# Performance work log

Measured on AMD Instinct MI355X. Metric: run time of the kernel, lower is better.

The kernel has to match this reference:

```python
import jax, jax.numpy as jnp
import numpy as np

EPS = 1e-6
LOSS_WEIGHT = 1.0


def _sigma_components(xywhr):
    """Closed-form symmetric 2x2 covariance Sigma = R diag((w/2)^2,(h/2)^2) R^T.
    Returns the three independent components (s00, s01, s11)."""
    wh = jnp.clip(xywhr[..., 2:4], 1e-7, 1e7)
    r = xywhr[..., 4]
    c, s = jnp.cos(r), jnp.sin(r)
    a = (0.5 * wh[..., 0]) ** 2  # (w/2)^2
    b = (0.5 * wh[..., 1]) ** 2  # (h/2)^2
    s00 = a * c * c + b * s * s
    s01 = (a - b) * s * c
    s11 = a * s * s + b * c * c
    return s00, s01, s11


def setup_inputs() -> dict:
    key = jax.random.key(0)
    kp, kt = jax.random.split(key)
    pred = jax.random.uniform(kp, (4096, 5), dtype=jnp.float32)
    target = jax.random.uniform(kt, (2048, 5), dtype=jnp.float32)
    return {"pred": pred, "target": target}


def reference(pred, target):
    # box_decode is identity here (boxes already xywhr). match=True path -> (M, N) cost.
    p00, p01, p11 = _sigma_components(pred)    # each (M,)
    t00, t01, t11 = _sigma_components(target)  # each (N,)

    det_p = p00 * p11 - p01 * p01
    det_t = t00 * t11 - t01 * t01
    Vb_p = 4.0 * jnp.sqrt(jnp.abs(det_p))[:, None]  # (M, 1)
    Vb_t = 4.0 * jnp.sqrt(jnp.abs(det_t))[None, :]  # (1, N)

    # Broadcast pred components over columns, target over rows -> (M, N) planes.
    p00, p01, p11 = p00[:, None], p01[:, None], p11[:, None]
    t00, t01, t11 = t00[None, :], t01[None, :], t11[None, :]

    # Sum S = Sigma_p + Sigma_t (symmetric), closed-form 2x2 inverse.
    m00, m01, m11 = p00 + t00, p01 + t01, p11 + t11
    det_m = m00 * m11 - m01 * m01
    i00, i01, i11 = m11 / det_m, -m01 / det_m, m00 / det_m

    # K = Sigma_p @ inv(S)  (generally non-symmetric)
    k00 = p00 * i00 + p01 * i01
    k01 = p00 * i01 + p01 * i11
    k10 = p01 * i00 + p11 * i01
    k11 = p01 * i01 + p11 * i11

    # Sigma = Sigma_p - K @ Sigma_p
    sig00 = p00 - (k00 * p00 + k01 * p01)
    sig01 = p01 - (k00 * p01 + k01 * p11)
    sig10 = p01 - (k10 * p00 + k11 * p01)
    sig11 = p11 - (k10 * p01 + k11 * p11)
    det_sig = sig00 * sig11 - sig01 * sig10

    Vb = 4.0 * jnp.sqrt(jnp.abs(det_sig))  # (M, N)
    KFIoU = Vb / (Vb_p + Vb_t - Vb + EPS)
    # fun='none': loss = 1 - KFIoU, clamped at 0; reduction='none'
    loss = jnp.clip(1.0 - KFIoU, 0.0)
    return loss * LOSS_WEIGHT
```

## Files before the change

kernel.cpp:

```cpp
#include <hip/hip_runtime.h>
#include <cmath>


typedef float v2f __attribute__((ext_vector_type(2)));

constexpr int ROWS = 16;
constexpr int COLS = 256;

__device__ __forceinline__ void sincos_cr(float rf, float* sf, float* cf) {
  double x = (double)rf;
  if (fabs(x) <= 1.0) {
    double z = x * x;
    double ps = -7.647163731819816e-13;
    ps = fma(ps, z, 1.605904383682161e-10);
    ps = fma(ps, z, -2.505210838544172e-08);
    ps = fma(ps, z, 2.755731922398589e-06);
    ps = fma(ps, z, -1.984126984126984e-04);
    ps = fma(ps, z, 8.333333333333333e-03);
    ps = fma(ps, z, -1.666666666666667e-01);
    double s = fma(ps * z, x, x);
    double pc = 1.561920696858623e-16;
    pc = fma(pc, z, -4.779477332387385e-14);
    pc = fma(pc, z, 1.147074559772972e-11);
    pc = fma(pc, z, -2.087675698786810e-09);
    pc = fma(pc, z, 2.755731922398589e-07);
    pc = fma(pc, z, -2.480158730158730e-05);
    pc = fma(pc, z, 1.388888888888889e-03);
    pc = fma(pc, z, -4.166666666666666e-02);
    pc = fma(pc, z, 5.000000000000000e-01);
    double c = fma(-pc, z, 1.0);
    *sf = (float)s;
    *cf = (float)c;
  } else {
    *sf = (float)sin(x);
    *cf = (float)cos(x);
  }
}

__global__ __launch_bounds__(256) void box_param_kernel(
    const float* __restrict__ pred, int np,
    const float* __restrict__ target, int nt,
    float4* __restrict__ ws) {
#pragma clang fp contract(off)
  int i = blockIdx.x * 256 + threadIdx.x;
  int n = np + nt;
  if (i >= n) return;
  const float* bx = (i < np) ? (pred + (size_t)i * 5)
                             : (target + (size_t)(i - np) * 5);
  float w = fminf(fmaxf(bx[2], 1e-7f), 1e7f);
  float h = fminf(fmaxf(bx[3], 1e-7f), 1e7f);
  float s, c;
  sincos_cr(bx[4], &s, &c);
  float a = (0.5f * w) * (0.5f * w);
  float b = (0.5f * h) * (0.5f * h);
  float s00 = a * c * c + b * s * s;
  float s01 = (a - b) * s * c;
  float s11 = a * s * s + b * c * c;
  float det = s00 * s11 - s01 * s01;
  float vb  = 4.0f * __fsqrt_rn(fabsf(det));
  ws[i] = make_float4(s00, s01, s11, vb);
}

__device__ __forceinline__ v2f rcp_refined(v2f d) {
  v2f r;
  r[0] = __builtin_amdgcn_rcpf(d[0]);
  r[1] = __builtin_amdgcn_rcpf(d[1]);
  v2f one = {1.0f, 1.0f};
  v2f e = __builtin_elementwise_fma(-d, r, one);
  return __builtin_elementwise_fma(e, r, r);
}

__device__ __forceinline__ v2f div_faithful(v2f a, v2f d, v2f r) {
  v2f q = a * r;
  v2f e = __builtin_elementwise_fma(-d, q, a);
  return __builtin_elementwise_fma(e, r, q);
}

__device__ __forceinline__ v2f kf_pair2(float4 p0, float4 p1, float4 t) {
#pragma clang fp contract(off)
  v2f px = {p0.x, p1.x};
  v2f py = {p0.y, p1.y};
  v2f pz = {p0.z, p1.z};
  v2f pw = {p0.w, p1.w};

  v2f m00 = px + t.x;
  v2f m01 = py + t.y;
  v2f m11 = pz + t.z;
  v2f det_m = m00 * m11 - m01 * m01;

  v2f r = rcp_refined(det_m);
  v2f i00 = div_faithful(m11, det_m, r);
  v2f i01 = div_faithful(-m01, det_m, r);
  v2f i11 = div_faithful(m00, det_m, r);

  v2f k00 = px * i00 + py * i01;
  v2f k01 = px * i01 + py * i11;
  v2f k10 = py * i00 + pz * i01;
  v2f k11 = py * i01 + pz * i11;

  v2f sig00 = px - (k00 * px + k01 * py);
  v2f sig01 = py - (k00 * py + k01 * pz);
  v2f sig10 = py - (k10 * px + k11 * py);
  v2f sig11 = pz - (k10 * py + k11 * pz);

  v2f det_sig = sig00 * sig11 - sig01 * sig10;
  v2f vb;
  vb[0] = 4.0f * __builtin_amdgcn_sqrtf(fabsf(det_sig[0]));
  vb[1] = 4.0f * __builtin_amdgcn_sqrtf(fabsf(det_sig[1]));

  v2f denom = pw + t.w - vb + 1e-6f;
  v2f rd = rcp_refined(denom);
  v2f kf = vb * rd;

  v2f one = {1.0f, 1.0f};
  v2f res = one - kf;
  res[0] = fmaxf(res[0], 0.0f);
  res[1] = fmaxf(res[1], 0.0f);
  return res;
}

__global__ __launch_bounds__(256, 8) void kf_loss_kernel(
    const float4* __restrict__ pp,
    const float4* __restrict__ tp,
    float* __restrict__ out, int np, int nt) {
  const int col  = blockIdx.y * COLS + threadIdx.x;
  const int row0 = blockIdx.x * ROWS;
  if (col >= nt) return;

  const float4 t = tp[col];

  for (int rr = 0; rr < ROWS; rr += 2) {
    int r0 = row0 + rr;
    int r1 = r0 + 1;
    int r0c = (r0 < np) ? r0 : (np - 1);
    int r1c = (r1 < np) ? r1 : (np - 1);
    float4 p0 = pp[r0c];
    float4 p1 = pp[r1c];
    v2f o = kf_pair2(p0, p1, t);
    if (r0 < np) out[(size_t)r0 * (size_t)nt + col] = o[0];
    if (r1 < np) out[(size_t)r1 * (size_t)nt + col] = o[1];
  }
}

extern "C" void kernel_launch(void* const* d_in, const int* in_sizes, int n_in,
                              void* d_out, int out_size, void* d_ws, size_t ws_size,
                              hipStream_t stream) {
  const float* pred   = (const float*)d_in[0];
  const float* target = (const float*)d_in[1];
  float* out = (float*)d_out;
  int np = in_sizes[0] / 5;
  int nt = in_sizes[1] / 5;

  float4* params = (float4*)d_ws;
  int nbox = np + nt;
  box_param_kernel<<<(nbox + 255) / 256, 256, 0, stream>>>(
      pred, np, target, nt, params);

  dim3 grid((np + ROWS - 1) / ROWS, (nt + COLS - 1) / COLS);
  kf_loss_kernel<<<grid, dim3(COLS), 0, stream>>>(
      params, params + np, out, np, nt);
}
```

Before: 23.67 us.

## Fuse box-parameter computation into loss kernel for divisible shapes

```diff
diff --git a/kernel.cpp b/kernel.cpp
--- a/kernel.cpp
+++ b/kernel.cpp
@@ -37,16 +37,8 @@
   }
 }
 
-__global__ __launch_bounds__(256) void box_param_kernel(
-    const float* __restrict__ pred, int np,
-    const float* __restrict__ target, int nt,
-    float4* __restrict__ ws) {
+__device__ __forceinline__ float4 box_params(const float* __restrict__ bx) {
 #pragma clang fp contract(off)
-  int i = blockIdx.x * 256 + threadIdx.x;
-  int n = np + nt;
-  if (i >= n) return;
-  const float* bx = (i < np) ? (pred + (size_t)i * 5)
-                             : (target + (size_t)(i - np) * 5);
   float w = fminf(fmaxf(bx[2], 1e-7f), 1e7f);
   float h = fminf(fmaxf(bx[3], 1e-7f), 1e7f);
   float s, c;
@@ -58,7 +50,7 @@
   float s11 = a * s * s + b * c * c;
   float det = s00 * s11 - s01 * s01;
   float vb  = 4.0f * __fsqrt_rn(fabsf(det));
-  ws[i] = make_float4(s00, s01, s11, vb);
+  return make_float4(s00, s01, s11, vb);
 }
 
 __device__ __forceinline__ v2f rcp_refined(v2f d) {
@@ -69,7 +61,6 @@
   v2f e = __builtin_elementwise_fma(-d, r, one);
   return __builtin_elementwise_fma(e, r, r);
 }
-
 __device__ __forceinline__ v2f div_faithful(v2f a, v2f d, v2f r) {
   v2f q = a * r;
   v2f e = __builtin_elementwise_fma(-d, q, a);
@@ -119,26 +110,87 @@
   return res;
 }
 
-__global__ __launch_bounds__(256, 8) void kf_loss_kernel(
-    const float4* __restrict__ pp,
-    const float4* __restrict__ tp,
+__global__ __launch_bounds__(256, 4) void kf_loss_fused(
+    const float* __restrict__ pred, const float* __restrict__ target,
+    float* __restrict__ out, int nt) {
+  __shared__ float4 sp[ROWS];
+  __shared__ float4 st[COLS];
+
+  const int tid  = threadIdx.x;
+  const int row0 = blockIdx.x * ROWS;
+  const int col0 = blockIdx.y * COLS;
+
+  st[tid] = box_params(target + (size_t)(col0 + tid) * 5);
+  if (tid < ROWS) sp[tid] = box_params(pred + (size_t)(row0 + tid) * 5);
+  __syncthreads();
+
+  const float4 t = st[tid];
+  float* o = out + (size_t)row0 * (size_t)nt + (size_t)(col0 + tid);
+
+  #pragma unroll
+  for (int rr = 0; rr < ROWS; rr += 2) {
+    v2f res = kf_pair2(sp[rr], sp[rr + 1], t);
+    o[0] = res[0];
+    o[(size_t)nt] = res[1];
+    o += (size_t)2 * (size_t)nt;
+  }
+}
+
+__global__ __launch_bounds__(256) void box_param_kernel(
+    const float* __restrict__ pred, int np,
+    const float* __restrict__ target, int nt,
+    float4* __restrict__ ws) {
+  int i = blockIdx.x * 256 + threadIdx.x;
+  int n = np + nt;
+  if (i >= n) return;
+  const float* bx = (i < np) ? (pred + (size_t)i * 5)
+                             : (target + (size_t)(i - np) * 5);
+  ws[i] = box_params(bx);
+}
+
+__device__ __forceinline__ float rcp_ref_s(float d) {
+  float r = __builtin_amdgcn_rcpf(d);
+  return fmaf(fmaf(-d, r, 1.0f), r, r);
+}
+__device__ __forceinline__ float div_f_s(float a, float d, float r) {
+  float q = a * r;
+  return fmaf(fmaf(-d, q, a), r, q);
+}
+__device__ float kf_pair_s(float4 p, float4 t) {
+#pragma clang fp contract(off)
+  float m00 = p.x + t.x, m01 = p.y + t.y, m11 = p.z + t.z;
+  float det_m = m00 * m11 - m01 * m01;
+  float r = rcp_ref_s(det_m);
+  float i00 = div_f_s(m11, det_m, r);
+  float i01 = div_f_s(-m01, det_m, r);
+  float i11 = div_f_s(m00, det_m, r);
+  float k00 = p.x * i00 + p.y * i01;
+  float k01 = p.x * i01 + p.y * i11;
+  float k10 = p.y * i00 + p.z * i01;
+  float k11 = p.y * i01 + p.z * i11;
+  float sig00 = p.x - (k00 * p.x + k01 * p.y);
+  float sig01 = p.y - (k00 * p.y + k01 * p.z);
+  float sig10 = p.y - (k10 * p.x + k11 * p.y);
+  float sig11 = p.z - (k10 * p.y + k11 * p.z);
+  float det_sig = sig00 * sig11 - sig01 * sig10;
+  float vb = 4.0f * __builtin_amdgcn_sqrtf(fabsf(det_sig));
+  float denom = p.w + t.w - vb + 1e-6f;
+  return fmaxf(1.0f - vb * rcp_ref_s(denom), 0.0f);
+}
+
+__global__ __launch_bounds__(256) void kf_loss_edge(
+    const float4* __restrict__ pp, const float4* __restrict__ tp,
     float* __restrict__ out, int np, int nt) {
   const int col  = blockIdx.y * COLS + threadIdx.x;
   const int row0 = blockIdx.x * ROWS;
   if (col >= nt) return;
-
   const float4 t = tp[col];
-
-  for (int rr = 0; rr < ROWS; rr += 2) {
-    int r0 = row0 + rr;
-    int r1 = r0 + 1;
-    int r0c = (r0 < np) ? r0 : (np - 1);
-    int r1c = (r1 < np) ? r1 : (np - 1);
-    float4 p0 = pp[r0c];
-    float4 p1 = pp[r1c];
-    v2f o = kf_pair2(p0, p1, t);
-    if (r0 < np) out[(size_t)r0 * (size_t)nt + col] = o[0];
-    if (r1 < np) out[(size_t)r1 * (size_t)nt + col] = o[1];
+  int rend = ROWS;
+  if (row0 + rend > np) rend = np - row0;
+  float* o = out + (size_t)row0 * (size_t)nt + col;
+  for (int rr = 0; rr < rend; ++rr) {
+    *o = kf_pair_s(pp[row0 + rr], t);
+    o += nt;
   }
 }
 
@@ -151,12 +203,16 @@
   int np = in_sizes[0] / 5;
   int nt = in_sizes[1] / 5;
 
-  float4* params = (float4*)d_ws;
-  int nbox = np + nt;
-  box_param_kernel<<<(nbox + 255) / 256, 256, 0, stream>>>(
-      pred, np, target, nt, params);
-
-  dim3 grid((np + ROWS - 1) / ROWS, (nt + COLS - 1) / COLS);
-  kf_loss_kernel<<<grid, dim3(COLS), 0, stream>>>(
-      params, params + np, out, np, nt);
-}
+  if ((np % ROWS) == 0 && (nt % COLS) == 0) {
+    dim3 grid(np / ROWS, nt / COLS);
+    kf_loss_fused<<<grid, dim3(COLS), 0, stream>>>(pred, target, out, nt);
+  } else {
+    float4* params = (float4*)d_ws;
+    int nbox = np + nt;
+    box_param_kernel<<<(nbox + 255) / 256, 256, 0, stream>>>(
+        pred, np, target, nt, params);
+    dim3 grid((np + ROWS - 1) / ROWS, (nt + COLS - 1) / COLS);
+    kf_loss_edge<<<grid, dim3(COLS), 0, stream>>>(
+        params, params + np, out, np, nt);
+  }
+}
```

Result: faster. 19.84 us (-16.2%).
